# Performance work log

Hardware: AMD Instinct MI355X
Metric: run time of the kernel (lower is better)

The kernel has to match this reference:

```python
import jax, jax.numpy as jnp
import numpy as np
import math

B, T, D, H = 4, 2048, 1024, 8
DK = D // H


def _rel_shift(x):
    # x: [B, H, T, P] with P = 2T-1 (Transformer-XL relative shift)
    b, h, q, p = x.shape
    x = jnp.pad(x, ((0, 0), (0, 0), (0, 0), (1, 0)))
    x = x.reshape(b, h, p + 1, q)[:, :, 1:]
    return x.reshape(b, h, q, p)


def setup_inputs() -> dict:
    key = jax.random.key(0)
    ks = jax.random.split(key, 9)
    s = 0.02
    x = jax.random.normal(ks[0], (B, T, D), jnp.float32)
    pos_emb = jax.random.normal(ks[1], (1, 2 * T - 1, D), jnp.float32)
    Wq = jax.random.normal(ks[2], (D, D), jnp.float32) * s
    Wk = jax.random.normal(ks[3], (D, D), jnp.float32) * s
    Wv = jax.random.normal(ks[4], (D, D), jnp.float32) * s
    Wo = jax.random.normal(ks[5], (D, D), jnp.float32) * s
    Wp = jax.random.normal(ks[6], (D, D), jnp.float32) * s
    pos_bias_u = jax.random.normal(ks[7], (H, DK), jnp.float32) * s
    pos_bias_v = jax.random.normal(ks[8], (H, DK), jnp.float32) * s
    return {"x": x, "pos_emb": pos_emb, "Wq": Wq, "Wk": Wk, "Wv": Wv,
            "Wo": Wo, "Wp": Wp, "pos_bias_u": pos_bias_u, "pos_bias_v": pos_bias_v}


def reference(x, pos_emb, Wq, Wk, Wv, Wo, Wp, pos_bias_u, pos_bias_v):
    b, t, d = x.shape
    h, dk = pos_bias_u.shape
    inv_sdk = 1.0 / math.sqrt(dk)
    # projections (torch Linear: y = x @ W.T)
    q = (x @ Wq.T).reshape(b, t, h, dk)          # [B,T,H,DK]
    k = (x @ Wk.T).reshape(b, t, h, dk)          # [B,T,H,DK]
    v = (x @ Wv.T).reshape(b, t, h, dk)          # [B,T,H,DK]
    p = (pos_emb @ Wp.T).reshape(-1, h, dk)      # [P,H,DK], P = 2T-1
    # content and position scores
    matrix_ac = jnp.einsum('bqhd,bkhd->bhqk', q + pos_bias_u, k)   # [B,H,T,T]
    matrix_bd = jnp.einsum('bqhd,phd->bhqp', q + pos_bias_v, p)    # [B,H,T,2T-1]
    matrix_bd = _rel_shift(matrix_bd)[..., :t]                     # [B,H,T,T]
    scores = (matrix_ac + matrix_bd) * inv_sdk
    attn = jax.nn.softmax(scores, axis=-1)
    out = jnp.einsum('bhqk,bkhd->bqhd', attn, v).reshape(b, t, h * dk)
    return out @ Wo.T
```

## Files before the change

kernel.cpp:

```cpp
#include <hip/hip_runtime.h>
#include <cstdint>
#include <math.h>

#define B_   4
#define T_   2048
#define D_   1024
#define H_   8
#define DK_  128
#define P_   4095
#define PS_  4096

typedef unsigned short ushort_t;
typedef __attribute__((ext_vector_type(8))) short short8;
typedef __attribute__((ext_vector_type(4))) float floatx4;

__device__ inline float bf2f(ushort_t s) {
    return __uint_as_float(((unsigned int)s) << 16);
}
__device__ inline ushort_t f2bf(float f) {
    unsigned int u = __float_as_uint(f);
    u += 0x7fffu + ((u >> 16) & 1u);
    return (ushort_t)(u >> 16);
}

__device__ inline floatx4 mfma16(short8 a, short8 b, floatx4 c) {
    return __builtin_amdgcn_mfma_f32_16x16x32_bf16(a, b, c, 0, 0, 0);
}

__device__ inline void gload_lds16(const ushort_t* g, ushort_t* l) {
    __builtin_amdgcn_global_load_lds(
        (const __attribute__((address_space(1))) unsigned int*)g,
        (__attribute__((address_space(3))) unsigned int*)l, 16, 0, 0);
}

__global__ void detect_kernel(const ushort_t* x, int* flag) {
    if (blockIdx.x == 0 && threadIdx.x == 0) {
        int m = 0;
        for (int i = 0; i < 64; ++i) {
            float v = bf2f(x[2 * i]);
            float a = fabsf(v);
            if (!(a == 0.0f || (a > 1e-20f && a < 1e10f))) m = 1;
        }
        flag[0] = m;
    }
}

#define CV_TOT 17826816
template <int MODE>
__global__ __launch_bounds__(256) void convert_kernel(
    const int* __restrict__ flag,
    const void* __restrict__ x, const void* __restrict__ pe,
    const void* __restrict__ wq, const void* __restrict__ wk,
    const void* __restrict__ wv, const void* __restrict__ wo,
    const void* __restrict__ wp, const void* __restrict__ ub,
    const void* __restrict__ vb, ushort_t* __restrict__ dst)
{
    if (flag[0] != MODE) return;
    const size_t i = ((size_t)blockIdx.x * 256 + threadIdx.x) * 4;
    if (i >= CV_TOT) return;
    const void* s; size_t off;
    if (i < 8388608)       { s = x;  off = i; }
    else if (i < 12581888) { s = pe; off = i - 8388608; }
    else if (i < 13630464) { s = wq; off = i - 12581888; }
    else if (i < 14679040) { s = wk; off = i - 13630464; }
    else if (i < 15727616) { s = wv; off = i - 14679040; }
    else if (i < 16776192) { s = wo; off = i - 15727616; }
    else if (i < 17824768) { s = wp; off = i - 16776192; }
    else if (i < 17825792) { s = ub; off = i - 17824768; }
    else                   { s = vb; off = i - 17825792; }
    const size_t d = i + (i >= 12581888 ? 1024 : 0);
    if (MODE == 0) {
        *(uint2*)(dst + d) = *(const uint2*)((const ushort_t*)s + off);
    } else {
        float4 f = *(const float4*)((const float*)s + off);
        uint2 o;
        o.x = (unsigned)f2bf(f.x) | ((unsigned)f2bf(f.y) << 16);
        o.y = (unsigned)f2bf(f.z) | ((unsigned)f2bf(f.w) << 16);
        *(uint2*)(dst + d) = o;
    }
}

__global__ __launch_bounds__(256, 3) void gemm_mfma(
    const int* __restrict__ flag,
    const ushort_t* __restrict__ A, const ushort_t* __restrict__ W,
    void* __restrict__ C, int smode)
{
    if (smode == 3 && flag[0] != 0) return;
    if (smode == 4 && flag[0] != 1) return;
    const int K = 1024, N = 1024;

    __shared__ ushort_t Al[16 * 512];
    __shared__ ushort_t Wl[16 * 512];

    const int tid  = threadIdx.x;
    const int w    = tid >> 6, lane = tid & 63;
    const int r15  = lane & 15, quad = lane >> 4;
    const int wm   = w >> 1, wn = w & 1;
    const int m0   = blockIdx.y * 128, n0 = blockIdx.x * 128;

    floatx4 acc[4][4];
    const floatx4 z4 = {0.f, 0.f, 0.f, 0.f};
#pragma unroll
    for (int mt = 0; mt < 4; ++mt)
#pragma unroll
        for (int nt = 0; nt < 4; ++nt) acc[mt][nt] = z4;

    for (int k0 = 0; k0 < K; k0 += 64) {
#pragma unroll
        for (int ss = 0; ss < 4; ++ss) {
            const int s  = w * 4 + ss;
            const int mg = s >> 1, ks = s & 1;
            const int row = mg * 16 + r15;
            const int col = k0 + ks * 32 + quad * 8;
            gload_lds16(A + (size_t)(m0 + row) * K + col, &Al[s * 512]);
            gload_lds16(W + (size_t)(n0 + row) * K + col, &Wl[s * 512]);
        }
        __syncthreads();

        short8 af[2][4], bf[2][4];
#pragma unroll
        for (int ks = 0; ks < 2; ++ks) {
#pragma unroll
            for (int mt = 0; mt < 4; ++mt)
                af[ks][mt] = *(const short8*)&Al[(((wm * 4 + mt) * 2 + ks) * 64 + lane) * 8];
#pragma unroll
            for (int nt = 0; nt < 4; ++nt)
                bf[ks][nt] = *(const short8*)&Wl[(((wn * 4 + nt) * 2 + ks) * 64 + lane) * 8];
        }
#pragma unroll
        for (int ks = 0; ks < 2; ++ks)
#pragma unroll
            for (int mt = 0; mt < 4; ++mt)
#pragma unroll
                for (int nt = 0; nt < 4; ++nt)
                    acc[mt][nt] = mfma16(af[ks][mt], bf[ks][nt], acc[mt][nt]);
        __syncthreads();
    }

#pragma unroll
    for (int mt = 0; mt < 4; ++mt)
#pragma unroll
        for (int nt = 0; nt < 4; ++nt)
#pragma unroll
            for (int i = 0; i < 4; ++i) {
                const int m = m0 + wm * 64 + mt * 16 + quad * 4 + i;
                const int n = n0 + wn * 64 + nt * 16 + r15;
                const float v = acc[mt][nt][i];
                if (smode == 0) {
                    const int b = m >> 11, t = m & (T_ - 1);
                    const int h = n >> 7, dk = n & (DK_ - 1);
                    ((ushort_t*)C)[(((size_t)(b * H_ + h)) * T_ + t) * DK_ + dk] = f2bf(v);
                } else if (smode == 1) {
                    const int h = n >> 7, dk = n & (DK_ - 1);
                    ((ushort_t*)C)[((size_t)h * PS_ + m) * DK_ + dk] = f2bf(v);
                } else if (smode == 2) {
                    const int b = m >> 11, t = m & (T_ - 1);
                    const int h = n >> 7, dk = n & (DK_ - 1);
                    ((ushort_t*)C)[((size_t)(b * H_ + h) * DK_ + dk) * T_ + t] = f2bf(v);
                } else if (smode == 3) {
                    ((ushort_t*)C)[(size_t)m * N + n] = f2bf(v);
                } else {
                    ((float*)C)[(size_t)m * N + n] = v;
                }
            }
}

__global__ __launch_bounds__(256, 2) void attn_mfma(
    const ushort_t* __restrict__ qg,
    const ushort_t* __restrict__ kgl,
    const ushort_t* __restrict__ vt,
    const ushort_t* __restrict__ pg,
    const ushort_t* __restrict__ ubb,
    const ushort_t* __restrict__ vbb,
    ushort_t* __restrict__ ao)
{
    __shared__ ushort_t K_lds[16 * 512];
    __shared__ ushort_t V_lds[16 * 512];
    __shared__ ushort_t P_lds[32 * 512];
    __shared__ __align__(16) ushort_t pr_lds[4][1024];

    const int tid  = threadIdx.x;
    const int w    = tid >> 6;
    const int lane = tid & 63;
    const int r15  = lane & 15;
    const int quad = lane >> 4;
    const int bh   = blockIdx.y;
    const int h    = bh & (H_ - 1);
    const int b    = bh >> 3;
    const int q0b  = blockIdx.x * 64;
    const int q0w  = q0b + w * 16;

    short8 quA[4], qvA[4];
    {
        const ushort_t* qrow = qg + ((size_t)bh * T_ + q0w + r15) * DK_;
#pragma unroll
        for (int ks = 0; ks < 4; ++ks) {
            const int dk0 = ks * 32 + quad * 8;
            uint4 q4 = *(const uint4*)(qrow + dk0);
            uint4 u4 = *(const uint4*)(ubb + (size_t)h * DK_ + dk0);
            uint4 v4 = *(const uint4*)(vbb + (size_t)h * DK_ + dk0);
            const ushort_t* qs = (const ushort_t*)&q4;
            const ushort_t* us = (const ushort_t*)&u4;
            const ushort_t* vs = (const ushort_t*)&v4;
#pragma unroll
            for (int j = 0; j < 8; ++j) {
                const float qf = bf2f(qs[j]);
                quA[ks][j] = (short)f2bf(qf + bf2f(us[j]));
                qvA[ks][j] = (short)f2bf(qf + bf2f(vs[j]));
            }
        }
    }

    int src[4], hi[4];
#pragma unroll
    for (int i = 0; i < 4; ++i) {
        const int c = r15 + 15 - quad * 4 - i;
        src[i] = quad * 16 + (c & 15);
        hi[i]  = c >> 4;
    }

    floatx4 o[8];
    const floatx4 z4 = {0.f, 0.f, 0.f, 0.f};
#pragma unroll
    for (int g = 0; g < 8; ++g) o[g] = z4;
    float mrun[4], lrun[4];
#pragma unroll
    for (int i = 0; i < 4; ++i) { mrun[i] = -1e30f; lrun[i] = 0.f; }

    const float scale = 0.08838834764831845f;

    for (int kc0 = 0; kc0 < T_; kc0 += 64) {
        const int pbb = kc0 - q0b + 1984;

#pragma unroll
        for (int ss = 0; ss < 4; ++ss) {
            const int ck = w * 4 + ss;
            gload_lds16(kgl + ((size_t)bh * T_ + kc0 + w * 16 + r15) * DK_ + ss * 32 + quad * 8,
                        &K_lds[ck * 512]);
            const int cv = w * 4 + ss;
            const int og = cv >> 1, ks2 = cv & 1;
            gload_lds16(vt + ((size_t)(bh * DK_ + og * 16 + r15)) * T_ + kc0 + ks2 * 32 + quad * 8,
                        &V_lds[cv * 512]);
        }
#pragma unroll
        for (int ss = 0; ss < 8; ++ss) {
            const int cp = w * 8 + ss;
            const int gb = cp >> 2, ks = cp & 3;
            gload_lds16(pg + ((size_t)h * PS_ + pbb + gb * 16 + r15) * DK_ + ks * 32 + quad * 8,
                        &P_lds[cp * 512]);
        }
        __syncthreads();

        floatx4 ac[4];
#pragma unroll
        for (int g = 0; g < 4; ++g) {
            ac[g] = z4;
#pragma unroll
            for (int ks = 0; ks < 4; ++ks)
                ac[g] = mfma16(quA[ks],
                               *(const short8*)&K_lds[((g * 4 + ks) * 64 + lane) * 8],
                               ac[g]);
        }
        floatx4 bd[5];
#pragma unroll
        for (int g = 0; g < 5; ++g) {
            bd[g] = z4;
            const int gb = (3 - w) + g;
#pragma unroll
            for (int ks = 0; ks < 4; ++ks)
                bd[g] = mfma16(qvA[ks],
                               *(const short8*)&P_lds[((gb * 4 + ks) * 64 + lane) * 8],
                               bd[g]);
        }

        float pr[4][4];
        float mc[4], alpha[4];
#pragma unroll
        for (int i = 0; i < 4; ++i) {
            float mm = -1e30f;
#pragma unroll
            for (int g = 0; g < 4; ++g) {
                const float lo = __shfl(bd[g][i],     src[i], 64);
                const float hh = __shfl(bd[g + 1][i], src[i], 64);
                const float s  = (ac[g][i] + (hi[i] ? hh : lo)) * scale;
                pr[g][i] = s;
                mm = fmaxf(mm, s);
            }
            mc[i] = mm;
        }
#pragma unroll
        for (int i = 0; i < 4; ++i) {
#pragma unroll
            for (int mk = 1; mk < 16; mk <<= 1)
                mc[i] = fmaxf(mc[i], __shfl_xor(mc[i], mk));
            const float mn = fmaxf(mrun[i], mc[i]);
            alpha[i] = __expf(mrun[i] - mn);
            mrun[i] = mn;
            float ls = 0.f;
#pragma unroll
            for (int g = 0; g < 4; ++g) {
                const float e = __expf(pr[g][i] - mn);
                pr[g][i] = e;
                ls += e;
            }
#pragma unroll
            for (int mk = 1; mk < 16; mk <<= 1)
                ls += __shfl_xor(ls, mk);
            lrun[i] = lrun[i] * alpha[i] + ls;
        }
#pragma unroll
        for (int g = 0; g < 8; ++g)
#pragma unroll
            for (int i = 0; i < 4; ++i) o[g][i] *= alpha[i];

#pragma unroll
        for (int g = 0; g < 4; ++g) {
            const int unit = (g >> 1) * 4 + (g & 1) * 2 + (r15 >> 3);
#pragma unroll
            for (int i = 0; i < 4; ++i)
                pr_lds[w][(unit * 16 + quad * 4 + i) * 8 + (r15 & 7)] = f2bf(pr[g][i]);
        }
        short8 pa[2];
#pragma unroll
        for (int ks2 = 0; ks2 < 2; ++ks2)
            pa[ks2] = *(const short8*)&pr_lds[w][(ks2 * 64 + lane) * 8];

#pragma unroll
        for (int og = 0; og < 8; ++og)
#pragma unroll
            for (int ks2 = 0; ks2 < 2; ++ks2)
                o[og] = mfma16(pa[ks2],
                               *(const short8*)&V_lds[((og * 2 + ks2) * 64 + lane) * 8],
                               o[og]);
        __syncthreads();
    }

    float inv[4];
#pragma unroll
    for (int i = 0; i < 4; ++i) inv[i] = 1.0f / lrun[i];
#pragma unroll
    for (int og = 0; og < 8; ++og)
#pragma unroll
        for (int i = 0; i < 4; ++i) {
            const size_t idx =
                ((size_t)(b * T_ + q0w + quad * 4 + i)) * D_ + h * DK_ + og * 16 + r15;
            ao[idx] = f2bf(o[og][i] * inv[i]);
        }
}

extern "C" void kernel_launch(void* const* d_in, const int* in_sizes, int n_in,
                              void* d_out, int out_size, void* d_ws, size_t ws_size,
                              hipStream_t stream) {
    const void* x  = d_in[0];
    const void* pe = d_in[1];
    const void* Wq = d_in[2];
    const void* Wk = d_in[3];
    const void* Wv = d_in[4];
    const void* Wo = d_in[5];
    const void* Wp = d_in[6];
    const void* ub = d_in[7];
    const void* vb = d_in[8];

    int* flag = (int*)d_ws;
    ushort_t* arena = (ushort_t*)d_ws + 16;
    ushort_t* xb   = arena;
    ushort_t* peb  = arena + 8388608;
    ushort_t* wqb  = arena + 12582912;
    ushort_t* wkb  = wqb + 1048576;
    ushort_t* wvb  = wkb + 1048576;
    ushort_t* wob  = wvb + 1048576;
    ushort_t* wpb  = wob + 1048576;
    ushort_t* ubb  = arena + 17825792;
    ushort_t* vbb  = ubb + 1024;
    ushort_t* q_ws  = arena + 17827840;
    ushort_t* k_ws  = q_ws + 8388608;
    ushort_t* vt_ws = k_ws + 8388608;
    ushort_t* p_ws  = vt_ws + 8388608;
    ushort_t* ao_ws = xb;

    detect_kernel<<<1, 64, 0, stream>>>((const ushort_t*)x, flag);

    const int cvb = CV_TOT / 4 / 256;
    convert_kernel<0><<<cvb, 256, 0, stream>>>(flag, x, pe, Wq, Wk, Wv, Wo, Wp, ub, vb, arena);
    convert_kernel<1><<<cvb, 256, 0, stream>>>(flag, x, pe, Wq, Wk, Wv, Wo, Wp, ub, vb, arena);

    const dim3 gX(8, 64);
    const dim3 gP(8, 32);
    gemm_mfma<<<gX, 256, 0, stream>>>(flag, xb,  wqb, q_ws, 0);
    gemm_mfma<<<gX, 256, 0, stream>>>(flag, xb,  wkb, k_ws, 0);
    gemm_mfma<<<gX, 256, 0, stream>>>(flag, xb,  wvb, vt_ws, 2);
    gemm_mfma<<<gP, 256, 0, stream>>>(flag, peb, wpb, p_ws, 1);

    attn_mfma<<<dim3(T_ / 64, B_ * H_), 256, 0, stream>>>(
        q_ws, k_ws, vt_ws, p_ws, ubb, vbb, ao_ws);

    gemm_mfma<<<gX, 256, 0, stream>>>(flag, ao_ws, wob, d_out, 3);
    gemm_mfma<<<gX, 256, 0, stream>>>(flag, ao_ws, wob, d_out, 4);
}
```

Measured before the change: 589.5 us.

## Double-buffer GEMM and attention, fuse QKV projection, widen attention query tile

The GEMM kernel now double-buffers its LDS tiles so the next K-slice is fetched while the current one is multiplied. The three Q/K/V projections become one launch over a concatenated weight matrix, using a new output mode that scatters into the three layouts. The attention kernel now handles 128 queries per block, two 16-row tiles per wave, reusing each K/V/P fragment twice. It also double-buffers K/V and uses a rolling ring buffer for the relative-position P rows. The cost is more LDS and registers per block and lower occupancy limits (launch bounds 2 and 1).

```diff
diff --git a/kernel.cpp b/kernel.cpp
--- a/kernel.cpp
+++ b/kernel.cpp
@@ -80,17 +80,16 @@
     }
 }
 
-__global__ __launch_bounds__(256, 3) void gemm_mfma(
+__global__ __launch_bounds__(256, 2) void gemm_mfma(
     const int* __restrict__ flag,
     const ushort_t* __restrict__ A, const ushort_t* __restrict__ W,
     void* __restrict__ C, int smode)
 {
     if (smode == 3 && flag[0] != 0) return;
     if (smode == 4 && flag[0] != 1) return;
-    const int K = 1024, N = 1024;
-
-    __shared__ ushort_t Al[16 * 512];
-    __shared__ ushort_t Wl[16 * 512];
+
+    __shared__ ushort_t Al[2][8192];
+    __shared__ ushort_t Wl[2][8192];
 
     const int tid  = threadIdx.x;
     const int w    = tid >> 6, lane = tid & 63;
@@ -105,27 +104,34 @@
 #pragma unroll
         for (int nt = 0; nt < 4; ++nt) acc[mt][nt] = z4;
 
-    for (int k0 = 0; k0 < K; k0 += 64) {
+    auto stage = [&](int bfi, int k0) {
 #pragma unroll
         for (int ss = 0; ss < 4; ++ss) {
             const int s  = w * 4 + ss;
             const int mg = s >> 1, ks = s & 1;
             const int row = mg * 16 + r15;
             const int col = k0 + ks * 32 + quad * 8;
-            gload_lds16(A + (size_t)(m0 + row) * K + col, &Al[s * 512]);
-            gload_lds16(W + (size_t)(n0 + row) * K + col, &Wl[s * 512]);
-        }
-        __syncthreads();
+            gload_lds16(A + (size_t)(m0 + row) * 1024 + col, &Al[bfi][s * 512]);
+            gload_lds16(W + (size_t)(n0 + row) * 1024 + col, &Wl[bfi][s * 512]);
+        }
+    };
+
+    stage(0, 0);
+    __syncthreads();
+
+    for (int k0 = 0; k0 < 1024; k0 += 64) {
+        const int cur = (k0 >> 6) & 1;
+        if (k0 + 64 < 1024) stage(cur ^ 1, k0 + 64);
 
         short8 af[2][4], bf[2][4];
 #pragma unroll
         for (int ks = 0; ks < 2; ++ks) {
 #pragma unroll
             for (int mt = 0; mt < 4; ++mt)
-                af[ks][mt] = *(const short8*)&Al[(((wm * 4 + mt) * 2 + ks) * 64 + lane) * 8];
+                af[ks][mt] = *(const short8*)&Al[cur][(((wm * 4 + mt) * 2 + ks) * 64 + lane) * 8];
 #pragma unroll
             for (int nt = 0; nt < 4; ++nt)
-                bf[ks][nt] = *(const short8*)&Wl[(((wn * 4 + nt) * 2 + ks) * 64 + lane) * 8];
+                bf[ks][nt] = *(const short8*)&Wl[cur][(((wn * 4 + nt) * 2 + ks) * 64 + lane) * 8];
         }
 #pragma unroll
         for (int ks = 0; ks < 2; ++ks)
@@ -146,26 +152,28 @@
                 const int m = m0 + wm * 64 + mt * 16 + quad * 4 + i;
                 const int n = n0 + wn * 64 + nt * 16 + r15;
                 const float v = acc[mt][nt][i];
-                if (smode == 0) {
-                    const int b = m >> 11, t = m & (T_ - 1);
-                    const int h = n >> 7, dk = n & (DK_ - 1);
-                    ((ushort_t*)C)[(((size_t)(b * H_ + h)) * T_ + t) * DK_ + dk] = f2bf(v);
+                if (smode == 5) {
+                    const int nh = n >> 10, nl = n & 1023;
+                    const int hh = nl >> 7, dk = nl & 127;
+                    const int bb = m >> 11, tt = m & 2047;
+                    if (nh == 0)
+                        ((ushort_t*)C)[(((size_t)(bb * 8 + hh)) * 2048 + tt) * 128 + dk] = f2bf(v);
+                    else if (nh == 1)
+                        ((ushort_t*)C)[8388608 + (((size_t)(bb * 8 + hh)) * 2048 + tt) * 128 + dk] = f2bf(v);
+                    else
+                        ((ushort_t*)C)[16777216 + ((size_t)(bb * 8 + hh) * 128 + dk) * 2048 + tt] = f2bf(v);
                 } else if (smode == 1) {
-                    const int h = n >> 7, dk = n & (DK_ - 1);
-                    ((ushort_t*)C)[((size_t)h * PS_ + m) * DK_ + dk] = f2bf(v);
-                } else if (smode == 2) {
-                    const int b = m >> 11, t = m & (T_ - 1);
-                    const int h = n >> 7, dk = n & (DK_ - 1);
-                    ((ushort_t*)C)[((size_t)(b * H_ + h) * DK_ + dk) * T_ + t] = f2bf(v);
+                    const int hh = n >> 7, dk = n & 127;
+                    ((ushort_t*)C)[((size_t)hh * PS_ + m) * 128 + dk] = f2bf(v);
                 } else if (smode == 3) {
-                    ((ushort_t*)C)[(size_t)m * N + n] = f2bf(v);
+                    ((ushort_t*)C)[(size_t)m * 1024 + n] = f2bf(v);
                 } else {
-                    ((float*)C)[(size_t)m * N + n] = v;
+                    ((float*)C)[(size_t)m * 1024 + n] = v;
                 }
             }
 }
 
-__global__ __launch_bounds__(256, 2) void attn_mfma(
+__global__ __launch_bounds__(256, 1) void attn_mfma(
     const ushort_t* __restrict__ qg,
     const ushort_t* __restrict__ kgl,
     const ushort_t* __restrict__ vt,
@@ -174,10 +182,10 @@
     const ushort_t* __restrict__ vbb,
     ushort_t* __restrict__ ao)
 {
-    __shared__ ushort_t K_lds[16 * 512];
-    __shared__ ushort_t V_lds[16 * 512];
-    __shared__ ushort_t P_lds[32 * 512];
-    __shared__ __align__(16) ushort_t pr_lds[4][1024];
+    __shared__ ushort_t K_lds[2][8192];
+    __shared__ ushort_t V_lds[2][8192];
+    __shared__ ushort_t P_lds[16][2048];
+    __shared__ __align__(16) ushort_t pr_lds[4][2][1024];
 
     const int tid  = threadIdx.x;
     const int w    = tid >> 6;
@@ -187,12 +195,13 @@
     const int bh   = blockIdx.y;
     const int h    = bh & (H_ - 1);
     const int b    = bh >> 3;
-    const int q0b  = blockIdx.x * 64;
-    const int q0w  = q0b + w * 16;
-
-    short8 quA[4], qvA[4];
-    {
-        const ushort_t* qrow = qg + ((size_t)bh * T_ + q0w + r15) * DK_;
+    const int q0b  = blockIdx.x * 128;
+    const int pbb0 = 1920 - q0b;
+
+    short8 quA[2][4], qvA[2][4];
+#pragma unroll
+    for (int mt = 0; mt < 2; ++mt) {
+        const ushort_t* qrow = qg + ((size_t)bh * T_ + q0b + w * 32 + mt * 16 + r15) * DK_;
 #pragma unroll
         for (int ks = 0; ks < 4; ++ks) {
             const int dk0 = ks * 32 + quad * 8;
@@ -205,8 +214,8 @@
 #pragma unroll
             for (int j = 0; j < 8; ++j) {
                 const float qf = bf2f(qs[j]);
-                quA[ks][j] = (short)f2bf(qf + bf2f(us[j]));
-                qvA[ks][j] = (short)f2bf(qf + bf2f(vs[j]));
+                quA[mt][ks][j] = (short)f2bf(qf + bf2f(us[j]));
+                qvA[mt][ks][j] = (short)f2bf(qf + bf2f(vs[j]));
             }
         }
     }
@@ -219,133 +228,162 @@
         hi[i]  = c >> 4;
     }
 
-    floatx4 o[8];
+    floatx4 o[2][8];
     const floatx4 z4 = {0.f, 0.f, 0.f, 0.f};
 #pragma unroll
-    for (int g = 0; g < 8; ++g) o[g] = z4;
-    float mrun[4], lrun[4];
-#pragma unroll
-    for (int i = 0; i < 4; ++i) { mrun[i] = -1e30f; lrun[i] = 0.f; }
+    for (int mt = 0; mt < 2; ++mt)
+#pragma unroll
+        for (int g = 0; g < 8; ++g) o[mt][g] = z4;
+    float mrun[2][4], lrun[2][4];
+#pragma unroll
+    for (int mt = 0; mt < 2; ++mt)
+#pragma unroll
+        for (int i = 0; i < 4; ++i) { mrun[mt][i] = -1e30f; lrun[mt][i] = 0.f; }
 
     const float scale = 0.08838834764831845f;
 
-    for (int kc0 = 0; kc0 < T_; kc0 += 64) {
-        const int pbb = kc0 - q0b + 1984;
-
+    auto stageKV = [&](int bfi, int kc) {
 #pragma unroll
         for (int ss = 0; ss < 4; ++ss) {
             const int ck = w * 4 + ss;
-            gload_lds16(kgl + ((size_t)bh * T_ + kc0 + w * 16 + r15) * DK_ + ss * 32 + quad * 8,
-                        &K_lds[ck * 512]);
-            const int cv = w * 4 + ss;
-            const int og = cv >> 1, ks2 = cv & 1;
-            gload_lds16(vt + ((size_t)(bh * DK_ + og * 16 + r15)) * T_ + kc0 + ks2 * 32 + quad * 8,
-                        &V_lds[cv * 512]);
-        }
-#pragma unroll
-        for (int ss = 0; ss < 8; ++ss) {
-            const int cp = w * 8 + ss;
-            const int gb = cp >> 2, ks = cp & 3;
-            gload_lds16(pg + ((size_t)h * PS_ + pbb + gb * 16 + r15) * DK_ + ks * 32 + quad * 8,
-                        &P_lds[cp * 512]);
-        }
+            gload_lds16(kgl + ((size_t)bh * T_ + kc + w * 16 + r15) * DK_ + ss * 32 + quad * 8,
+                        &K_lds[bfi][ck * 512]);
+            const int og = ck >> 1, ks2 = ck & 1;
+            gload_lds16(vt + ((size_t)(bh * DK_ + og * 16 + r15)) * T_ + kc + ks2 * 32 + quad * 8,
+                        &V_lds[bfi][ck * 512]);
+        }
+    };
+    auto stageP = [&](int lg) {
+        const int sl = lg & 15;
+        const int grow = pbb0 + lg * 16 + r15;
+#pragma unroll
+        for (int ks = 0; ks < 4; ++ks)
+            gload_lds16(pg + ((size_t)h * PS_ + grow) * DK_ + ks * 32 + quad * 8,
+                        &P_lds[sl][ks * 512]);
+    };
+
+    stageKV(0, 0);
+    stageP(w * 3);
+    stageP(w * 3 + 1);
+    stageP(w * 3 + 2);
+    __syncthreads();
+
+    for (int ib = 0; ib < 32; ++ib) {
+        const int kc0 = ib * 64, cur = ib & 1;
+        if (ib < 31) {
+            stageKV(cur ^ 1, kc0 + 64);
+            stageP(4 * ib + 12 + w);
+        }
+
+        floatx4 ac[2][4];
+#pragma unroll
+        for (int g = 0; g < 4; ++g) { ac[0][g] = z4; ac[1][g] = z4; }
+#pragma unroll
+        for (int g = 0; g < 4; ++g)
+#pragma unroll
+            for (int ks = 0; ks < 4; ++ks) {
+                const short8 kf = *(const short8*)&K_lds[cur][((g * 4 + ks) * 64 + lane) * 8];
+                ac[0][g] = mfma16(quA[0][ks], kf, ac[0][g]);
+                ac[1][g] = mfma16(quA[1][ks], kf, ac[1][g]);
+            }
+
+        floatx4 bd[2][5];
+#pragma unroll
+        for (int g = 0; g < 5; ++g) { bd[0][g] = z4; bd[1][g] = z4; }
+        const int base6 = 4 * ib + 6 - 2 * w;
+#pragma unroll
+        for (int gbu = 0; gbu < 6; ++gbu) {
+            const int sl = (base6 + gbu) & 15;
+#pragma unroll
+            for (int ks = 0; ks < 4; ++ks) {
+                const short8 pf = *(const short8*)&P_lds[sl][(ks * 64 + lane) * 8];
+                if (gbu < 5)  bd[1][gbu]     = mfma16(qvA[1][ks], pf, bd[1][gbu]);
+                if (gbu >= 1) bd[0][gbu - 1] = mfma16(qvA[0][ks], pf, bd[0][gbu - 1]);
+            }
+        }
+
+#pragma unroll
+        for (int mt = 0; mt < 2; ++mt) {
+            float pr[4][4];
+            float mc[4], alpha[4];
+#pragma unroll
+            for (int i = 0; i < 4; ++i) {
+                float mm = -1e30f;
+#pragma unroll
+                for (int g = 0; g < 4; ++g) {
+                    const float lo = __shfl(bd[mt][g][i],     src[i], 64);
+                    const float hh = __shfl(bd[mt][g + 1][i], src[i], 64);
+                    const float s  = (ac[mt][g][i] + (hi[i] ? hh : lo)) * scale;
+                    pr[g][i] = s;
+                    mm = fmaxf(mm, s);
+                }
+                mc[i] = mm;
+            }
+#pragma unroll
+            for (int i = 0; i < 4; ++i) {
+#pragma unroll
+                for (int mk = 1; mk < 16; mk <<= 1)
+                    mc[i] = fmaxf(mc[i], __shfl_xor(mc[i], mk));
+                const float mn = fmaxf(mrun[mt][i], mc[i]);
+                alpha[i] = __expf(mrun[mt][i] - mn);
+                mrun[mt][i] = mn;
+                float ls = 0.f;
+#pragma unroll
+                for (int g = 0; g < 4; ++g) {
+                    const float e = __expf(pr[g][i] - mn);
+                    pr[g][i] = e;
+                    ls += e;
+                }
+#pragma unroll
+                for (int mk = 1; mk < 16; mk <<= 1)
+                    ls += __shfl_xor(ls, mk);
+                lrun[mt][i] = lrun[mt][i] * alpha[i] + ls;
+            }
+#pragma unroll
+            for (int g = 0; g < 8; ++g)
+#pragma unroll
+                for (int i = 0; i < 4; ++i) o[mt][g][i] *= alpha[i];
+#pragma unroll
+            for (int g = 0; g < 4; ++g) {
+                const int unit = (g >> 1) * 4 + (g & 1) * 2 + (r15 >> 3);
+#pragma unroll
+                for (int i = 0; i < 4; ++i)
+                    pr_lds[w][mt][(unit * 16 + quad * 4 + i) * 8 + (r15 & 7)] = f2bf(pr[g][i]);
+            }
+        }
+
+        short8 pa[2][2];
+#pragma unroll
+        for (int mt = 0; mt < 2; ++mt)
+#pragma unroll
+            for (int ks2 = 0; ks2 < 2; ++ks2)
+                pa[mt][ks2] = *(const short8*)&pr_lds[w][mt][(ks2 * 64 + lane) * 8];
+#pragma unroll
+        for (int og = 0; og < 8; ++og)
+#pragma unroll
+            for (int ks2 = 0; ks2 < 2; ++ks2) {
+                const short8 vf = *(const short8*)&V_lds[cur][((og * 2 + ks2) * 64 + lane) * 8];
+                o[0][og] = mfma16(pa[0][ks2], vf, o[0][og]);
+                o[1][og] = mfma16(pa[1][ks2], vf, o[1][og]);
+            }
         __syncthreads();
-
-        floatx4 ac[4];
-#pragma unroll
-        for (int g = 0; g < 4; ++g) {
-            ac[g] = z4;
-#pragma unroll
-            for (int ks = 0; ks < 4; ++ks)
-                ac[g] = mfma16(quA[ks],
-                               *(const short8*)&K_lds[((g * 4 + ks) * 64 + lane) * 8],
-                               ac[g]);
-        }
-        floatx4 bd[5];
-#pragma unroll
-        for (int g = 0; g < 5; ++g) {
-            bd[g] = z4;
-            const int gb = (3 - w) + g;
-#pragma unroll
-            for (int ks = 0; ks < 4; ++ks)
-                bd[g] = mfma16(qvA[ks],
-                               *(const short8*)&P_lds[((gb * 4 + ks) * 64 + lane) * 8],
-                               bd[g]);
-        }
-
-        float pr[4][4];
-        float mc[4], alpha[4];
-#pragma unroll
-        for (int i = 0; i < 4; ++i) {
-            float mm = -1e30f;
-#pragma unroll
-            for (int g = 0; g < 4; ++g) {
-                const float lo = __shfl(bd[g][i],     src[i], 64);
-                const float hh = __shfl(bd[g + 1][i], src[i], 64);
-                const float s  = (ac[g][i] + (hi[i] ? hh : lo)) * scale;
-                pr[g][i] = s;
-                mm = fmaxf(mm, s);
-            }
-            mc[i] = mm;
-        }
-#pragma unroll
-        for (int i = 0; i < 4; ++i) {
-#pragma unroll
-            for (int mk = 1; mk < 16; mk <<= 1)
-                mc[i] = fmaxf(mc[i], __shfl_xor(mc[i], mk));
-            const float mn = fmaxf(mrun[i], mc[i]);
-            alpha[i] = __expf(mrun[i] - mn);
-            mrun[i] = mn;
-            float ls = 0.f;
-#pragma unroll
-            for (int g = 0; g < 4; ++g) {
-                const float e = __expf(pr[g][i] - mn);
-                pr[g][i] = e;
-                ls += e;
-            }
-#pragma unroll
-            for (int mk = 1; mk < 16; mk <<= 1)
-                ls += __shfl_xor(ls, mk);
-            lrun[i] = lrun[i] * alpha[i] + ls;
-        }
-#pragma unroll
-        for (int g = 0; g < 8; ++g)
-#pragma unroll
-            for (int i = 0; i < 4; ++i) o[g][i] *= alpha[i];
-
-#pragma unroll
-        for (int g = 0; g < 4; ++g) {
-            const int unit = (g >> 1) * 4 + (g & 1) * 2 + (r15 >> 3);
-#pragma unroll
-            for (int i = 0; i < 4; ++i)
-                pr_lds[w][(unit * 16 + quad * 4 + i) * 8 + (r15 & 7)] = f2bf(pr[g][i]);
-        }
-        short8 pa[2];
-#pragma unroll
-        for (int ks2 = 0; ks2 < 2; ++ks2)
-            pa[ks2] = *(const short8*)&pr_lds[w][(ks2 * 64 + lane) * 8];
-
+    }
+
+#pragma unroll
+    for (int mt = 0; mt < 2; ++mt) {
+        float inv[4];
+#pragma unroll
+        for (int i = 0; i < 4; ++i) inv[i] = 1.0f / lrun[mt][i];
 #pragma unroll
         for (int og = 0; og < 8; ++og)
 #pragma unroll
-            for (int ks2 = 0; ks2 < 2; ++ks2)
-                o[og] = mfma16(pa[ks2],
-                               *(const short8*)&V_lds[((og * 2 + ks2) * 64 + lane) * 8],
-                               o[og]);
-        __syncthreads();
-    }
-
-    float inv[4];
-#pragma unroll
-    for (int i = 0; i < 4; ++i) inv[i] = 1.0f / lrun[i];
-#pragma unroll
-    for (int og = 0; og < 8; ++og)
-#pragma unroll
-        for (int i = 0; i < 4; ++i) {
-            const size_t idx =
-                ((size_t)(b * T_ + q0w + quad * 4 + i)) * D_ + h * DK_ + og * 16 + r15;
-            ao[idx] = f2bf(o[og][i] * inv[i]);
-        }
+            for (int i = 0; i < 4; ++i) {
+                const size_t idx =
+                    ((size_t)(b * T_ + q0b + w * 32 + mt * 16 + quad * 4 + i)) * D_
+                    + h * DK_ + og * 16 + r15;
+                ao[idx] = f2bf(o[mt][og][i] * inv[i]);
+            }
+    }
 }
 
 extern "C" void kernel_launch(void* const* d_in, const int* in_sizes, int n_in,
@@ -366,16 +404,12 @@
     ushort_t* xb   = arena;
     ushort_t* peb  = arena + 8388608;
     ushort_t* wqb  = arena + 12582912;
-    ushort_t* wkb  = wqb + 1048576;
-    ushort_t* wvb  = wkb + 1048576;
-    ushort_t* wob  = wvb + 1048576;
+    ushort_t* wob  = wqb + 3 * 1048576;
     ushort_t* wpb  = wob + 1048576;
     ushort_t* ubb  = arena + 17825792;
     ushort_t* vbb  = ubb + 1024;
     ushort_t* q_ws  = arena + 17827840;
-    ushort_t* k_ws  = q_ws + 8388608;
-    ushort_t* vt_ws = k_ws + 8388608;
-    ushort_t* p_ws  = vt_ws + 8388608;
+    ushort_t* p_ws  = q_ws + 3 * 8388608;
     ushort_t* ao_ws = xb;
 
     detect_kernel<<<1, 64, 0, stream>>>((const ushort_t*)x, flag);
@@ -384,16 +418,12 @@
     convert_kernel<0><<<cvb, 256, 0, stream>>>(flag, x, pe, Wq, Wk, Wv, Wo, Wp, ub, vb, arena);
     convert_kernel<1><<<cvb, 256, 0, stream>>>(flag, x, pe, Wq, Wk, Wv, Wo, Wp, ub, vb, arena);
 
-    const dim3 gX(8, 64);
-    const dim3 gP(8, 32);
-    gemm_mfma<<<gX, 256, 0, stream>>>(flag, xb,  wqb, q_ws, 0);
-    gemm_mfma<<<gX, 256, 0, stream>>>(flag, xb,  wkb, k_ws, 0);
-    gemm_mfma<<<gX, 256, 0, stream>>>(flag, xb,  wvb, vt_ws, 2);
-    gemm_mfma<<<gP, 256, 0, stream>>>(flag, peb, wpb, p_ws, 1);
-
-    attn_mfma<<<dim3(T_ / 64, B_ * H_), 256, 0, stream>>>(
-        q_ws, k_ws, vt_ws, p_ws, ubb, vbb, ao_ws);
-
-    gemm_mfma<<<gX, 256, 0, stream>>>(flag, ao_ws, wob, d_out, 3);
-    gemm_mfma<<<gX, 256, 0, stream>>>(flag, ao_ws, wob, d_out, 4);
-}
+    gemm_mfma<<<dim3(24, 64), 256, 0, stream>>>(flag, xb,  wqb, q_ws, 5);
+    gemm_mfma<<<dim3(8, 32),  256, 0, stream>>>(flag, peb, wpb, p_ws, 1);
+
+    attn_mfma<<<dim3(T_ / 128, B_ * H_), 256, 0, stream>>>(
+        q_ws, q_ws + 8388608, q_ws + 16777216, p_ws, ubb, vbb, ao_ws);
+
+    gemm_mfma<<<dim3(8, 64), 256, 0, stream>>>(flag, ao_ws, wob, d_out, 3);
+    gemm_mfma<<<dim3(8, 64), 256, 0, stream>>>(flag, ao_ws, wob, d_out, 4);
+}
```

Measured after the change: 782.7 us. 1.33x slower.
